# Optimization experiments

Hardware: AMD Instinct MI355X
Metric: run time of the kernel (lower is better)

The kernel has to match this reference:

```python
import jax, jax.numpy as jnp
import numpy as np

K = 5          # kernel_size per pseudo-dim
KK = K * K     # 25 weight slots (dim=2)
NUM_GRAPHS = 64


def spline_conv(x, src, dst, pseudo, W, root, bias):
    """SplineConv, degree-1 open B-spline, dim=2, aggr='mean', root weight + bias.
    x: [N, I], pseudo: [E, 2] in [0,1], W: [KK, I, O], root: [I, O], bias: [O].
    """
    N = x.shape[0]
    E = src.shape[0]
    O = W.shape[-1]
    # degree-1 open spline: v = u * (K-1); linear interpolation between knots
    v = pseudo * (K - 1)                      # [E, 2]
    bot = jnp.floor(v)
    frac = v - bot                            # [E, 2]
    bot = bot.astype(jnp.int32)
    # precompute per-node transform for every kernel slot: [N, KK, O] -> flat [N*KK, O]
    Xk = jnp.einsum('ni,kio->nko', x, W).reshape(N * KK, O)
    msg = jnp.zeros((E, O), x.dtype)
    for s0 in (0, 1):
        b0 = frac[:, 0] if s0 else 1.0 - frac[:, 0]
        i0 = jnp.clip(bot[:, 0] + s0, 0, K - 1)
        for s1 in (0, 1):
            b1 = frac[:, 1] if s1 else 1.0 - frac[:, 1]
            i1 = jnp.clip(bot[:, 1] + s1, 0, K - 1)
            flat = src * KK + i0 * K + i1     # [E] gather index into Xk
            msg = msg + (b0 * b1)[:, None] * Xk[flat]
    # mean aggregation over incoming edges
    agg = jax.ops.segment_sum(msg, dst, num_segments=N)
    deg = jax.ops.segment_sum(jnp.ones((E,), x.dtype), dst, num_segments=N)
    agg = agg / jnp.maximum(deg, 1.0)[:, None]
    return agg + x @ root + bias


def batch_average(x, batch, num_graphs):
    s = jax.ops.segment_sum(x, batch, num_segments=num_graphs)
    c = jax.ops.segment_sum(jnp.ones((x.shape[0],), x.dtype), batch, num_segments=num_graphs)
    return s / jnp.maximum(c, 1.0)[:, None]


def setup_inputs() -> dict:
    key = jax.random.key(0)
    ks = jax.random.split(key, 16)
    N, E = 30000, 600000
    x = jax.random.normal(ks[0], (N, 8), dtype=jnp.float32)
    edge_index = jax.random.randint(ks[1], (2, E), 0, N, dtype=jnp.int64)
    pseudo = jax.random.uniform(ks[2], (E, 2), dtype=jnp.float32)
    batch = jnp.sort(jax.random.randint(ks[3], (N,), 0, NUM_GRAPHS, dtype=jnp.int64))

    def glorot(k, shape):
        fan = shape[-2] + shape[-1]
        return jax.random.normal(k, shape, dtype=jnp.float32) * np.sqrt(2.0 / fan)

    return {
        'x': x, 'edge_index': edge_index, 'pseudo': pseudo, 'batch': batch,
        'W1': glorot(ks[4], (KK, 8, 32)),   'root1': glorot(ks[5], (8, 32)),   'b1': jnp.zeros((32,), jnp.float32),
        'W2': glorot(ks[6], (KK, 32, 64)),  'root2': glorot(ks[7], (32, 64)),  'b2': jnp.zeros((64,), jnp.float32),
        'W3': glorot(ks[8], (KK, 64, 124)), 'root3': glorot(ks[9], (64, 124)), 'b3': jnp.zeros((124,), jnp.float32),
        'fc_w': glorot(ks[10], (124, 30)),  'fc_b': jnp.zeros((30,), jnp.float32),
    }


def reference(x, edge_index, pseudo, batch,
              W1, root1, b1, W2, root2, b2, W3, root3, b3, fc_w, fc_b):
    src = edge_index[0].astype(jnp.int32)
    dst = edge_index[1].astype(jnp.int32)
    batch32 = batch.astype(jnp.int32)
    h = jax.nn.elu(spline_conv(x, src, dst, pseudo, W1, root1, b1))
    h = jax.nn.elu(spline_conv(h, src, dst, pseudo, W2, root2, b2))
    h = jax.nn.elu(spline_conv(h, src, dst, pseudo, W3, root3, b3))
    g = batch_average(h, batch32, NUM_GRAPHS)        # [G, 124]
    # dropout is identity in eval mode
    logits = g @ fc_w + fc_b                         # [G, 30]
    return jax.nn.log_softmax(logits, axis=-1)
```

## Files before the change

### kernel.cpp

```cpp
#include <hip/hip_runtime.h>
#include <cstdint>
#include <cstddef>

#define KKSLOTS 25

typedef __attribute__((ext_vector_type(8))) short short8;
typedef __attribute__((ext_vector_type(4))) float f32x4;
typedef __attribute__((ext_vector_type(4))) unsigned short us4;

__device__ __forceinline__ unsigned short f2bf(float f) {
    unsigned u = __float_as_uint(f);
    u += 0x7FFF + ((u >> 16) & 1);
    return (unsigned short)(u >> 16);
}
__device__ __forceinline__ float bf2f(unsigned short b) {
    return __uint_as_float((unsigned)b << 16);
}

__device__ __forceinline__ void gload16(const void* g, void* l) {
    __builtin_amdgcn_global_load_lds(
        (const __attribute__((address_space(1))) unsigned*)g,
        (__attribute__((address_space(3))) unsigned*)l, 16, 0, 0);
}

__global__ void csr_count_kernel(const int* __restrict__ dst, int* __restrict__ cnt, int E) {
    int e = blockIdx.x * blockDim.x + threadIdx.x;
    if (e < E) atomicAdd(&cnt[dst[e]], 1);
}

#define SCAN_B 256
__global__ __launch_bounds__(SCAN_B) void scan1_kernel(const int* __restrict__ cnt,
                                                       int* __restrict__ off,
                                                       int* __restrict__ bsum, int N) {
    __shared__ int tmp[SCAN_B];
    int g = blockIdx.x * SCAN_B + threadIdx.x;
    int v = (g < N) ? cnt[g] : 0;
    tmp[threadIdx.x] = v;
    __syncthreads();
    for (int d = 1; d < SCAN_B; d <<= 1) {
        int t = (threadIdx.x >= d) ? tmp[threadIdx.x - d] : 0;
        __syncthreads();
        tmp[threadIdx.x] += t;
        __syncthreads();
    }
    if (g < N) off[g] = tmp[threadIdx.x] - v;
    if (threadIdx.x == SCAN_B - 1) bsum[blockIdx.x] = tmp[threadIdx.x];
}

__global__ __launch_bounds__(SCAN_B) void scan2_kernel(int* __restrict__ bsum, int nb) {
    __shared__ int tmp[SCAN_B];
    int v = (threadIdx.x < nb) ? bsum[threadIdx.x] : 0;
    tmp[threadIdx.x] = v;
    __syncthreads();
    for (int d = 1; d < SCAN_B; d <<= 1) {
        int t = (threadIdx.x >= d) ? tmp[threadIdx.x - d] : 0;
        __syncthreads();
        tmp[threadIdx.x] += t;
        __syncthreads();
    }
    if (threadIdx.x < nb) bsum[threadIdx.x] = tmp[threadIdx.x] - v;
}

__global__ void scan3_kernel(int* __restrict__ off, const int* __restrict__ bsum, int N) {
    int g = blockIdx.x * SCAN_B + threadIdx.x;
    if (g < N) off[g] += bsum[blockIdx.x];
}

__global__ void csr_fill_kernel(const int* __restrict__ src, const int* __restrict__ dst,
                                const float* __restrict__ pseudo,
                                int* __restrict__ off, int4* __restrict__ rec, int E) {
    int e = blockIdx.x * blockDim.x + threadIdx.x;
    if (e >= E) return;
    int d = dst[e];
    int p = atomicAdd(&off[d], 1);
    float v0 = pseudo[2 * e + 0] * 4.0f;
    float v1 = pseudo[2 * e + 1] * 4.0f;
    float fl0 = floorf(v0), fl1 = floorf(v1);
    float f0 = v0 - fl0, f1 = v1 - fl1;
    int b0 = (int)fl0, b1 = (int)fl1;
    int i0a = min(max(b0, 0), 4),     i1a = min(max(b1, 0), 4);
    int i0b = min(max(b0 + 1, 0), 4), i1b = min(max(b1 + 1, 0), 4);
    int s00 = i0a * 5 + i1a;
    int s01 = i0a * 5 + i1b;
    int s10 = i0b * 5 + i1a;
    int s11 = i0b * 5 + i1b;
    int packed = s00 | (s01 << 5) | (s10 << 10) | (s11 << 15);
    int4 r;
    r.x = src[e];
    r.y = packed;
    r.z = __float_as_int(f0);
    r.w = __float_as_int(f1);
    rec[p] = r;
}

__global__ void to_bf16_kernel(const float* __restrict__ in, unsigned short* __restrict__ out, int n) {
    int i = blockIdx.x * 256 + threadIdx.x;
    if (i < n) out[i] = f2bf(in[i]);
}

template<int KP, int I, int O, int OP>
__global__ void build_wt_kernel(const float* __restrict__ W, const float* __restrict__ root,
                                unsigned short* __restrict__ WT) {
    int idx = blockIdx.x * 256 + threadIdx.x;
    if (idx >= OP * KP) return;
    int o = idx / KP, k = idx - o * KP;
    float v = 0.0f;
    if (o < O) {
        if (k < KKSLOTS * I) v = W[(size_t)k * O + o];
        else if (k < (KKSLOTS + 1) * I) v = root[(size_t)(k - KKSLOTS * I) * O + o];
    }
    WT[idx] = f2bf(v);
}

template<int I>
__device__ __forceinline__ void edge_add(float* la, int lane, int4 r,
                                         const unsigned short* __restrict__ xb) {
    float f0 = __int_as_float(r.z), f1 = __int_as_float(r.w);
    float g0 = 1.0f - f0, g1 = 1.0f - f1;
    int pk = r.y;
    if constexpr (I == 64) {
        float xv = bf2f(xb[(size_t)r.x * 64 + lane]);
        la[((pk      ) & 31) * 64 + lane] += g0 * g1 * xv;
        la[((pk >> 5 ) & 31) * 64 + lane] += g0 * f1 * xv;
        la[((pk >> 10) & 31) * 64 + lane] += f0 * g1 * xv;
        la[((pk >> 15) & 31) * 64 + lane] += f0 * f1 * xv;
    } else if constexpr (I == 32) {
        int ch = lane & 31, half = lane >> 5;
        float xv = bf2f(xb[(size_t)r.x * 32 + ch]);
        float wA = half ? f0 : g0;
        int sh = half * 10;
        int sA = (pk >> sh) & 31, sB = (pk >> (sh + 5)) & 31;
        la[sA * 32 + ch] += wA * g1 * xv;
        la[sB * 32 + ch] += wA * f1 * xv;
    } else {
        int ch = lane & 7, corner = (lane >> 3) & 3;
        if (lane < 32) {
            float xv = bf2f(xb[(size_t)r.x * 8 + ch]);
            int s = (pk >> (corner * 5)) & 31;
            float w = ((corner & 2) ? f0 : g0) * ((corner & 1) ? f1 : g1);
            la[s * 8 + ch] += w * xv;
        }
    }
}

template<int I, int KP>
__global__ __launch_bounds__(256) void seg_accum_kernel(
        const unsigned short* __restrict__ xb, const int4* __restrict__ rec,
        const int* __restrict__ off, unsigned short* __restrict__ accB,
        int nlo, int nhi) {
    constexpr int SLOTS = KKSLOTS * I;
    __shared__ float la_all[4][SLOTS];
    int wline = threadIdx.x >> 6, lane = threadIdx.x & 63;
    float* la = la_all[wline];
    int wid = blockIdx.x * 4 + wline;
    int nwt = gridDim.x << 2;

    int e_lo = (nlo == 0) ? 0 : off[nlo - 1];
    int e_hi = off[nhi - 1];
    long long span = (long long)e_hi - e_lo;
    int t0 = e_lo + (int)(span * wid / nwt);
    int t1 = e_lo + (int)(span * (wid + 1) / nwt);

    int ns, ne;
    {   int lo = nlo, hi = nhi;
        while (lo < hi) { int m = (lo + hi) >> 1; if (off[m] > t0) hi = m; else lo = m + 1; }
        ns = (wid == 0) ? nlo : lo; }
    {   int lo = nlo, hi = nhi;
        while (lo < hi) { int m = (lo + hi) >> 1; if (off[m] > t1) hi = m; else lo = m + 1; }
        ne = (wid == nwt - 1) ? nhi : lo; }
    if (ns >= ne) return;

    for (int t = lane; t < SLOTS; t += 64) la[t] = 0.0f;
    int j = (ns == 0) ? 0 : off[ns - 1];
    for (int n = ns; n < ne; ++n) {
        int je = off[n];
        int jstart = j;
        while (j + 4 <= je) {
            int4 r0 = rec[j], r1 = rec[j + 1], r2 = rec[j + 2], r3 = rec[j + 3];
            edge_add<I>(la, lane, r0, xb);
            edge_add<I>(la, lane, r1, xb);
            edge_add<I>(la, lane, r2, xb);
            edge_add<I>(la, lane, r3, xb);
            j += 4;
        }
        while (j < je) { edge_add<I>(la, lane, rec[j], xb); ++j; }

        float dinv = 1.0f / fmaxf((float)(je - jstart), 1.0f);
        unsigned short* drow = accB + (size_t)(n - nlo) * KP;
        for (int t = lane; t < SLOTS; t += 64) drow[t] = f2bf(la[t] * dinv);
        for (int t = SLOTS + lane; t < KP; t += 64) {
            int ii = t - SLOTS;
            drow[t] = (ii < I) ? xb[(size_t)n * I + ii] : (unsigned short)0;
        }
        for (int t = lane; t < SLOTS; t += 64) la[t] = 0.0f;
    }
}

template<int KP, int O, int OP>
__global__ __launch_bounds__(512) void contract_mfma_kernel(
        const unsigned short* __restrict__ accB, const unsigned short* __restrict__ WT,
        const float* __restrict__ bias, unsigned short* __restrict__ hout,
        int nlo, int nhi) {
    constexpr int OSUB = OP / 2;
    constexpr int NF = OSUB / 16;
    constexpr int NS = KP / 32;
    constexpr int BT = OP * 64;
    constexpr int AT = 64 * 64;
    __shared__ __attribute__((aligned(16))) char Bt[2][BT];
    __shared__ __attribute__((aligned(16))) char At[2][AT];

    int tid = threadIdx.x;
    int wv = tid >> 6, lane = tid & 63;
    int ng = wv & 3, oh = wv >> 2;
    int quad = lane >> 4, l16 = lane & 15;
    int n0 = nlo + blockIdx.x * 64;

    const char* WTc = (const char*)WT;
    const char* ACc = (const char*)accB;
    int pB = tid * 16;
    int rowB = pB >> 6;
    int colB = (pB & 63) ^ (((rowB >> 1) & 3) << 4);
    const char* bsrc = WTc + (size_t)rowB * (KP * 2) + colB;
    int pA = tid * 16;
    int rowA = pA >> 6;
    int arowA = min(n0 + rowA, nhi - 1) - nlo;
    int colA = (pA & 63) ^ (((rowA >> 1) & 3) << 4);
    const char* asrc = ACc + (size_t)arowA * (KP * 2) + colA;

    int rA = ng * 16 + l16;
    int aoff = rA * 64 + ((quad ^ ((rA >> 1) & 3)) << 4);
    int boff[NF];
    #pragma unroll
    for (int t = 0; t < NF; ++t) {
        int rB = oh * OSUB + t * 16 + l16;
        boff[t] = rB * 64 + ((quad ^ ((rB >> 1) & 3)) << 4);
    }

    f32x4 acc[NF];
    #pragma unroll
    for (int t = 0; t < NF; ++t) acc[t] = (f32x4){0.0f, 0.0f, 0.0f, 0.0f};

    auto STAGE = [&](int buf, int k0) {
        int kb = k0 * 2;
        if (pB < BT) gload16(bsrc + kb, &Bt[buf][wv << 10]);
        if (pA < AT) gload16(asrc + kb, &At[buf][wv << 10]);
    };

    STAGE(0, 0);
    __syncthreads();

    for (int s = 0; s < NS; ++s) {
        int cur = s & 1;
        if (s + 1 < NS) STAGE(cur ^ 1, (s + 1) * 32);
        short8 a = *(const short8*)(At[cur] + aoff);
        #pragma unroll
        for (int t = 0; t < NF; ++t) {
            short8 b = *(const short8*)(Bt[cur] + boff[t]);
            acc[t] = __builtin_amdgcn_mfma_f32_16x16x32_bf16(a, b, acc[t], 0, 0, 0);
        }
        __syncthreads();
    }

    #pragma unroll
    for (int t = 0; t < NF; ++t) {
        int o = oh * OSUB + t * 16 + l16;
        if (o >= O) continue;
        float bs = bias[o];
        #pragma unroll
        for (int r = 0; r < 4; ++r) {
            int n = n0 + ng * 16 + quad * 4 + r;
            if (n >= nhi) continue;
            float v = acc[t][r] + bs;
            v = (v > 0.0f) ? v : expm1f(v);
            hout[(size_t)n * OP + o] = f2bf(v);
        }
    }
}

#define GS_CH 128
__global__ __launch_bounds__(128) void graph_reduce_kernel(
        const unsigned short* __restrict__ h3, const int* __restrict__ batch,
        float* __restrict__ g, int N) {
    int o = threadIdx.x;
    if (o >= 124) return;
    int n0 = blockIdx.x * GS_CH;
    int n1 = min(n0 + GS_CH, N);
    float local = 0.0f;
    int cur_b = batch[n0];
    for (int n = n0; n < n1; ++n) {
        int b = batch[n];
        if (b != cur_b) {
            atomicAdd(&g[cur_b * 124 + o], local);
            local = 0.0f;
            cur_b = b;
        }
        local += bf2f(h3[(size_t)n * 128 + o]);
    }
    atomicAdd(&g[cur_b * 124 + o], local);
}

__global__ __launch_bounds__(256) void batch_count_kernel(
        const int* __restrict__ batch, float* __restrict__ cnt, int N) {
    __shared__ int hist[64];
    int tid = threadIdx.x;
    if (tid < 64) hist[tid] = 0;
    __syncthreads();
    int n = blockIdx.x * blockDim.x + tid;
    if (n < N) atomicAdd(&hist[batch[n]], 1);
    __syncthreads();
    if (tid < 64 && hist[tid] > 0) atomicAdd(&cnt[tid], (float)hist[tid]);
}

__global__ void head_kernel(const float* __restrict__ g, const float* __restrict__ cnt,
                            const float* __restrict__ fcw, const float* __restrict__ fcb,
                            float* __restrict__ out) {
    __shared__ float logits[32];
    __shared__ float red[2];
    int b = blockIdx.x;
    int o = threadIdx.x;
    float c = fmaxf(cnt[b], 1.0f);
    if (o < 30) {
        float a = fcb[o];
        for (int i = 0; i < 124; ++i)
            a = fmaf(g[b * 124 + i] / c, fcw[i * 30 + o], a);
        logits[o] = a;
    }
    __syncthreads();
    if (o == 0) {
        float m = -1e30f;
        for (int j = 0; j < 30; ++j) m = fmaxf(m, logits[j]);
        float s = 0.0f;
        for (int j = 0; j < 30; ++j) s += expf(logits[j] - m);
        red[0] = m;
        red[1] = logf(s);
    }
    __syncthreads();
    if (o < 30) out[b * 30 + o] = logits[o] - red[0] - red[1];
}

template<int I, int O, int OP>
static void run_layer(const unsigned short* hb, const unsigned short* WT, const float* bias,
                      unsigned short* hout, unsigned short* accB,
                      const int4* rec, const int* off,
                      int N, size_t avail, hipStream_t stream) {
    constexpr int KP = ((26 * I + 31) / 32) * 32;
    size_t perNode = (size_t)KP * 2;
    size_t maxNodesS = avail / perNode;
    int maxNodes = (maxNodesS > (size_t)N) ? N : (int)maxNodesS;
    maxNodes &= ~63;
    if (maxNodes < 64) maxNodes = 64;
    for (int nlo = 0; nlo < N; nlo += maxNodes) {
        int nhi = nlo + maxNodes;
        if (nhi > N) nhi = N;
        int cn = nhi - nlo;
        seg_accum_kernel<I, KP><<<1024, 256, 0, stream>>>(hb, rec, off, accB, nlo, nhi);
        contract_mfma_kernel<KP, O, OP><<<(cn + 63) / 64, 512, 0, stream>>>(
            accB, WT, bias, hout, nlo, nhi);
    }
}

extern "C" void kernel_launch(void* const* d_in, const int* in_sizes, int n_in,
                              void* d_out, int out_size, void* d_ws, size_t ws_size,
                              hipStream_t stream) {
    const float* x      = (const float*)d_in[0];
    const int*   ei     = (const int*)  d_in[1];
    const float* pseudo = (const float*)d_in[2];
    const int*   batch  = (const int*)  d_in[3];
    const float* W1 = (const float*)d_in[4];
    const float* r1 = (const float*)d_in[5];
    const float* b1 = (const float*)d_in[6];
    const float* W2 = (const float*)d_in[7];
    const float* r2 = (const float*)d_in[8];
    const float* b2 = (const float*)d_in[9];
    const float* W3 = (const float*)d_in[10];
    const float* r3 = (const float*)d_in[11];
    const float* b3 = (const float*)d_in[12];
    const float* fcw = (const float*)d_in[13];
    const float* fcb = (const float*)d_in[14];

    int N = in_sizes[0] / 8;
    int E = in_sizes[1] / 2;
    const int* srcp = ei;
    const int* dstp = ei + E;

    constexpr int KP1 = 224, KP2 = 832, KP3 = 1664;

    char* p = (char*)d_ws;
    unsigned short* xb  = (unsigned short*)p; p += (size_t)N * 8 * 2;
    unsigned short* h1  = (unsigned short*)p; p += (size_t)N * 32 * 2;
    unsigned short* h2  = (unsigned short*)p; p += (size_t)N * 64 * 2;
    unsigned short* h3  = (unsigned short*)p; p += (size_t)N * 128 * 2;
    float* gbuf = (float*)p; p += 64 * 124 * 4;
    float* cntF = (float*)p; p += 256;
    int*   cntI = (int*)p;   p += ((size_t)N * 4 + 15) & ~15ULL;
    int*   off  = (int*)p;   p += ((size_t)N * 4 + 15) & ~15ULL;
    int*   bsum = (int*)p;   p += SCAN_B * 4;
    int4*  rec  = (int4*)p;  p += (size_t)E * 16;
    unsigned short* WT1 = (unsigned short*)p; p += (size_t)32  * KP1 * 2;
    unsigned short* WT2 = (unsigned short*)p; p += (size_t)64  * KP2 * 2;
    unsigned short* WT3 = (unsigned short*)p; p += (size_t)128 * KP3 * 2;
    unsigned short* accB = (unsigned short*)p;
    size_t used = (size_t)(p - (char*)d_ws);
    size_t avail = (ws_size > used) ? (ws_size - used) : 0;

    hipMemsetAsync(gbuf, 0, 64 * 124 * 4 + 256 + (((size_t)N * 4 + 15) & ~15ULL), stream);

    int nb_scan = (N + SCAN_B - 1) / SCAN_B;
    csr_count_kernel<<<(E + 255) / 256, 256, 0, stream>>>(dstp, cntI, E);
    scan1_kernel<<<nb_scan, SCAN_B, 0, stream>>>(cntI, off, bsum, N);
    scan2_kernel<<<1, SCAN_B, 0, stream>>>(bsum, nb_scan);
    scan3_kernel<<<nb_scan, SCAN_B, 0, stream>>>(off, bsum, N);
    csr_fill_kernel<<<(E + 255) / 256, 256, 0, stream>>>(srcp, dstp, pseudo, off, rec, E);

    to_bf16_kernel<<<(N * 8 + 255) / 256, 256, 0, stream>>>(x, xb, N * 8);
    build_wt_kernel<KP1, 8,  32,  32 ><<<(32  * KP1 + 255) / 256, 256, 0, stream>>>(W1, r1, WT1);
    build_wt_kernel<KP2, 32, 64,  64 ><<<(64  * KP2 + 255) / 256, 256, 0, stream>>>(W2, r2, WT2);
    build_wt_kernel<KP3, 64, 124, 128><<<(128 * KP3 + 255) / 256, 256, 0, stream>>>(W3, r3, WT3);

    run_layer<8,  32,  32 >(xb, WT1, b1, h1, accB, rec, off, N, avail, stream);
    run_layer<32, 64,  64 >(h1, WT2, b2, h2, accB, rec, off, N, avail, stream);
    run_layer<64, 124, 128>(h2, WT3, b3, h3, accB, rec, off, N, avail, stream);

    graph_reduce_kernel<<<(N + GS_CH - 1) / GS_CH, 128, 0, stream>>>(h3, batch, gbuf, N);
    batch_count_kernel<<<(N + 255) / 256, 256, 0, stream>>>(batch, cntF, N);
    head_kernel<<<64, 64, 0, stream>>>(gbuf, cntF, fcw, fcb, (float*)d_out);
}
```

Before: 518.3 us.

## Accumulate spline slot sums in registers via wave-uniform switch instead of LDS

The per-node 25-slot accumulator moves from LDS into per-lane registers. Each edge record now stores a single 4x4 base-cell index, so the wave takes that index with readfirstlane and a 16-way switch picks which four registers to update with the bilinear weights. The clamp to 0..3 keeps the four corners equivalent to the old clamped indices, and the grid is doubled to 2048 blocks. This removes LDS read-modify-write traffic and LDS capacity limits on occupancy, at the cost of per-edge branch overhead, higher register pressure, and idle lanes for the I=8 and I=32 layers.

```diff
diff --git a/kernel.cpp b/kernel.cpp
--- a/kernel.cpp
+++ b/kernel.cpp
@@ -77,17 +77,11 @@
     float v1 = pseudo[2 * e + 1] * 4.0f;
     float fl0 = floorf(v0), fl1 = floorf(v1);
     float f0 = v0 - fl0, f1 = v1 - fl1;
-    int b0 = (int)fl0, b1 = (int)fl1;
-    int i0a = min(max(b0, 0), 4),     i1a = min(max(b1, 0), 4);
-    int i0b = min(max(b0 + 1, 0), 4), i1b = min(max(b1 + 1, 0), 4);
-    int s00 = i0a * 5 + i1a;
-    int s01 = i0a * 5 + i1b;
-    int s10 = i0b * 5 + i1a;
-    int s11 = i0b * 5 + i1b;
-    int packed = s00 | (s01 << 5) | (s10 << 10) | (s11 << 15);
+    int b0 = min(max((int)fl0, 0), 3);
+    int b1 = min(max((int)fl1, 0), 3);
     int4 r;
     r.x = src[e];
-    r.y = packed;
+    r.y = b0 * 4 + b1;
     r.z = __float_as_int(f0);
     r.w = __float_as_int(f1);
     rec[p] = r;
@@ -113,33 +107,26 @@
 }
 
 template<int I>
-__device__ __forceinline__ void edge_add(float* la, int lane, int4 r,
-                                         const unsigned short* __restrict__ xb) {
+__device__ __forceinline__ float ldx(const unsigned short* __restrict__ xb, int src, int lane) {
+    int ch = lane & (I - 1);
+    float v = bf2f(xb[(size_t)src * I + ch]);
+    return (lane < I) ? v : 0.0f;
+}
+
+__device__ __forceinline__ void edge_acc(float acc[25], int4 r, float xv) {
     float f0 = __int_as_float(r.z), f1 = __int_as_float(r.w);
     float g0 = 1.0f - f0, g1 = 1.0f - f1;
-    int pk = r.y;
-    if constexpr (I == 64) {
-        float xv = bf2f(xb[(size_t)r.x * 64 + lane]);
-        la[((pk      ) & 31) * 64 + lane] += g0 * g1 * xv;
-        la[((pk >> 5 ) & 31) * 64 + lane] += g0 * f1 * xv;
-        la[((pk >> 10) & 31) * 64 + lane] += f0 * g1 * xv;
-        la[((pk >> 15) & 31) * 64 + lane] += f0 * f1 * xv;
-    } else if constexpr (I == 32) {
-        int ch = lane & 31, half = lane >> 5;
-        float xv = bf2f(xb[(size_t)r.x * 32 + ch]);
-        float wA = half ? f0 : g0;
-        int sh = half * 10;
-        int sA = (pk >> sh) & 31, sB = (pk >> (sh + 5)) & 31;
-        la[sA * 32 + ch] += wA * g1 * xv;
-        la[sB * 32 + ch] += wA * f1 * xv;
-    } else {
-        int ch = lane & 7, corner = (lane >> 3) & 3;
-        if (lane < 32) {
-            float xv = bf2f(xb[(size_t)r.x * 8 + ch]);
-            int s = (pk >> (corner * 5)) & 31;
-            float w = ((corner & 2) ? f0 : g0) * ((corner & 1) ? f1 : g1);
-            la[s * 8 + ch] += w * xv;
-        }
+    float w00 = g0 * g1, w01 = g0 * f1, w10 = f0 * g1, w11 = f0 * f1;
+    int idx = __builtin_amdgcn_readfirstlane(r.y);
+    switch (idx) {
+#define CC(B0,B1) case (B0*4+B1): \
+        acc[B0*5+B1  ] += w00 * xv; acc[B0*5+B1+1] += w01 * xv; \
+        acc[B0*5+B1+5] += w10 * xv; acc[B0*5+B1+6] += w11 * xv; break;
+        CC(0,0) CC(0,1) CC(0,2) CC(0,3)
+        CC(1,0) CC(1,1) CC(1,2) CC(1,3)
+        CC(2,0) CC(2,1) CC(2,2) CC(2,3)
+        CC(3,0) CC(3,1) CC(3,2) CC(3,3)
+#undef CC
     }
 }
 
@@ -149,9 +136,7 @@
         const int* __restrict__ off, unsigned short* __restrict__ accB,
         int nlo, int nhi) {
     constexpr int SLOTS = KKSLOTS * I;
-    __shared__ float la_all[4][SLOTS];
     int wline = threadIdx.x >> 6, lane = threadIdx.x & 63;
-    float* la = la_all[wline];
     int wid = blockIdx.x * 4 + wline;
     int nwt = gridDim.x << 2;
 
@@ -170,29 +155,45 @@
         ne = (wid == nwt - 1) ? nhi : lo; }
     if (ns >= ne) return;
 
-    for (int t = lane; t < SLOTS; t += 64) la[t] = 0.0f;
+    float acc[25];
+    #pragma unroll
+    for (int s = 0; s < 25; ++s) acc[s] = 0.0f;
+
     int j = (ns == 0) ? 0 : off[ns - 1];
     for (int n = ns; n < ne; ++n) {
         int je = off[n];
         int jstart = j;
         while (j + 4 <= je) {
             int4 r0 = rec[j], r1 = rec[j + 1], r2 = rec[j + 2], r3 = rec[j + 3];
-            edge_add<I>(la, lane, r0, xb);
-            edge_add<I>(la, lane, r1, xb);
-            edge_add<I>(la, lane, r2, xb);
-            edge_add<I>(la, lane, r3, xb);
+            float x0 = ldx<I>(xb, r0.x, lane);
+            float x1 = ldx<I>(xb, r1.x, lane);
+            float x2 = ldx<I>(xb, r2.x, lane);
+            float x3 = ldx<I>(xb, r3.x, lane);
+            edge_acc(acc, r0, x0);
+            edge_acc(acc, r1, x1);
+            edge_acc(acc, r2, x2);
+            edge_acc(acc, r3, x3);
             j += 4;
         }
-        while (j < je) { edge_add<I>(la, lane, rec[j], xb); ++j; }
+        while (j < je) {
+            int4 r = rec[j];
+            edge_acc(acc, r, ldx<I>(xb, r.x, lane));
+            ++j;
+        }
 
         float dinv = 1.0f / fmaxf((float)(je - jstart), 1.0f);
         unsigned short* drow = accB + (size_t)(n - nlo) * KP;
-        for (int t = lane; t < SLOTS; t += 64) drow[t] = f2bf(la[t] * dinv);
+        if (lane < I) {
+            #pragma unroll
+            for (int s = 0; s < 25; ++s)
+                drow[(size_t)s * I + lane] = f2bf(acc[s] * dinv);
+        }
         for (int t = SLOTS + lane; t < KP; t += 64) {
             int ii = t - SLOTS;
             drow[t] = (ii < I) ? xb[(size_t)n * I + ii] : (unsigned short)0;
         }
-        for (int t = lane; t < SLOTS; t += 64) la[t] = 0.0f;
+        #pragma unroll
+        for (int s = 0; s < 25; ++s) acc[s] = 0.0f;
     }
 }
 
@@ -353,7 +354,7 @@
         int nhi = nlo + maxNodes;
         if (nhi > N) nhi = N;
         int cn = nhi - nlo;
-        seg_accum_kernel<I, KP><<<1024, 256, 0, stream>>>(hb, rec, off, accB, nlo, nhi);
+        seg_accum_kernel<I, KP><<<2048, 256, 0, stream>>>(hb, rec, off, accB, nlo, nhi);
         contract_mfma_kernel<KP, O, OP><<<(cn + 63) / 64, 512, 0, stream>>>(
             accB, WT, bias, hout, nlo, nhi);
     }
```

Measured after the change: 862.8 us. +66.5%, slower.
